# Performance work log

Hardware: AMD Instinct MI355X
Metric: run time of the kernel (lower is better)

## Reference

```python
import jax, jax.numpy as jnp
import numpy as np

B, N, D, H, O = 256, 1024, 512, 2048, 512


def setup_inputs() -> dict:
    key = jax.random.key(0)
    ks = jax.random.split(key, 6)
    x = jax.random.normal(ks[0], (B, N, D), dtype=jnp.float32)
    # binary float mask [B,N,1]; ensure every set has >=1 unpadded element
    mask = (jax.random.uniform(ks[1], (B, N, 1)) < 0.9).astype(jnp.float32)
    mask = mask.at[:, :1, :].set(1.0)
    # per-row (4B rows after stat-concat) unpadded counts in [1, N]
    unpadded = jax.random.randint(ks[2], (4 * B, 1), 1, N + 1).astype(jnp.float32)
    W1 = jax.random.normal(ks[3], (D, H), dtype=jnp.float32) * (1.0 / np.sqrt(D))
    b1 = jnp.zeros((H,), jnp.float32)
    W2 = jax.random.normal(ks[4], (H, O), dtype=jnp.float32) * (1.0 / np.sqrt(H))
    b2 = jnp.zeros((O,), jnp.float32)
    return dict(x=x, mask=mask, unpadded=unpadded, W1=W1, b1=b1, W2=W2, b2=b2)


def reference(x, mask, unpadded, W1, b1, W2, b2):
    # x: [B,N,D], mask: [B,N,1] (0/1 float)
    neg_inf = jnp.float32(-jnp.inf)
    cnt = mask.sum(axis=1)                              # [B,1]
    mean = (x * mask).sum(axis=1) / cnt                 # [B,D]
    agg_max = jnp.where(mask > 0, x, neg_inf).max(axis=1)   # [B,D]
    agg_min = -jnp.where(mask > 0, -x, neg_inf).max(axis=1) # [B,D]
    var = (jnp.square(x - mean[:, None, :]) * mask).sum(axis=1) / cnt
    std = jnp.sqrt(var)                                 # [B,D]
    aggr = jnp.concatenate([mean, agg_max, agg_min, std], axis=0)  # [4B,D]
    # faithful to source: delta = sum(unpadded)/unpadded.shape[1] + 1 (scalar)
    delta = unpadded.sum() / unpadded.shape[1] + 1.0
    logu = jnp.log(unpadded + 1.0)                      # [4B,1]
    amplification = aggr * (logu / delta)
    attenuation = aggr * (delta / logu)
    scale_concat = jnp.concatenate([aggr, amplification, attenuation], axis=0)  # [12B,D]
    h = jax.nn.relu(scale_concat @ W1 + b1)
    return h @ W2 + b2                                  # [12B,O]
```

## Files before the change

kernel.cpp:

```cpp
#include <hip/hip_runtime.h>
#include <hip/hip_bf16.h>
#include <math.h>
#include <stdint.h>

#define B_  256
#define N_  1024
#define D_  512
#define H_  2048
#define O_  512
#define M4  (4 * B_)
#define M12 (12 * B_)
#define NCH 8

typedef __attribute__((ext_vector_type(8))) short short8;
typedef __attribute__((ext_vector_type(4))) float f32x4;
typedef unsigned short ushort_t;

__device__ inline uint32_t pkbf(float a, float b) {
    union { __hip_bfloat162 h; uint32_t u; } cv;
    cv.h = __float22bfloat162_rn(float2{a, b});
    return cv.u;
}
__device__ inline ushort_t f2bf(float f) {
    union { float f; uint32_t u; } v; v.f = f;
    uint32_t r = v.u + 0x7FFFu + ((v.u >> 16) & 1u);
    return (ushort_t)(r >> 16);
}

__device__ inline void load_lds16(const void* g, void* l) {
    typedef const __attribute__((address_space(1))) uint32_t* gp_t;
    typedef __attribute__((address_space(3))) uint32_t* lp_t;
    __builtin_amdgcn_global_load_lds((gp_t)(uintptr_t)g, (lp_t)(uint32_t)(uintptr_t)l,
                                     16, 0, 0);
}

__device__ __forceinline__ void agg_core(const float* __restrict__ x,
                                         const float* __restrict__ mask,
                                         float* __restrict__ part,
                                         float* __restrict__ cntp,
                                         int id, int t) {
    const int b    = id >> 2;
    const int c    = id & 3;
    const int half = t >> 7;
    const int d4   = (t & 127) << 2;
    const float* base = x + ((size_t)b * N_ + (size_t)c * 256) * D_ + d4;
    const float* mp   = mask + (size_t)b * N_ + (size_t)c * 256;

    f32x4 sum = {0.f,0.f,0.f,0.f}, sq = {0.f,0.f,0.f,0.f};
    f32x4 mx = {-INFINITY,-INFINITY,-INFINITY,-INFINITY};
    f32x4 mn = { INFINITY, INFINITY, INFINITY, INFINITY};
    float cnt = 0.f;

    #pragma unroll 8
    for (int n = half; n < 256; n += 2) {
        float m = mp[n];
        f32x4 v = __builtin_nontemporal_load((const f32x4*)(base + (size_t)n * D_));
        sum.x = fmaf(v.x, m, sum.x); sum.y = fmaf(v.y, m, sum.y);
        sum.z = fmaf(v.z, m, sum.z); sum.w = fmaf(v.w, m, sum.w);
        sq.x  = fmaf(v.x * v.x, m, sq.x); sq.y = fmaf(v.y * v.y, m, sq.y);
        sq.z  = fmaf(v.z * v.z, m, sq.z); sq.w = fmaf(v.w * v.w, m, sq.w);
        cnt  += m;
        bool um = m > 0.f;
        mx.x = um ? fmaxf(mx.x, v.x) : mx.x; mx.y = um ? fmaxf(mx.y, v.y) : mx.y;
        mx.z = um ? fmaxf(mx.z, v.z) : mx.z; mx.w = um ? fmaxf(mx.w, v.w) : mx.w;
        mn.x = um ? fminf(mn.x, v.x) : mn.x; mn.y = um ? fminf(mn.y, v.y) : mn.y;
        mn.z = um ? fminf(mn.z, v.z) : mn.z; mn.w = um ? fminf(mn.w, v.w) : mn.w;
    }

    const int ch = c * 2 + half;
    const size_t SS = (size_t)B_ * NCH * D_;
    const size_t pi = ((size_t)(b * NCH + ch)) * D_ + d4;
    *(f32x4*)(part + 0 * SS + pi) = sum;
    *(f32x4*)(part + 1 * SS + pi) = sq;
    *(f32x4*)(part + 2 * SS + pi) = mx;
    *(f32x4*)(part + 3 * SS + pi) = mn;
    if ((t & 127) == 0) cntp[b * NCH + ch] = cnt;
}

__device__ void conv_tile(const float* __restrict__ in, ushort_t* __restrict__ out,
                          int R, int C, int bx, int by, float* tile ) {
    const int t  = threadIdx.x;
    const int r0 = by << 5;
    const int c0 = bx << 5;
    const int tr = t >> 3;
    const int tc = (t & 7) << 2;

    float4 v = *(const float4*)(in + (size_t)(r0 + tr) * C + c0 + tc);
    tile[tr * 33 + tc + 0] = v.x; tile[tr * 33 + tc + 1] = v.y;
    tile[tr * 33 + tc + 2] = v.z; tile[tr * 33 + tc + 3] = v.w;
    __syncthreads();

    union { uint32_t u[2]; ushort4 us; } o;
    o.u[0] = pkbf(tile[(tc + 0) * 33 + tr], tile[(tc + 1) * 33 + tr]);
    o.u[1] = pkbf(tile[(tc + 2) * 33 + tr], tile[(tc + 3) * 33 + tr]);
    *(ushort4*)(out + (size_t)(c0 + tr) * R + r0 + tc) = o.us;
}

__global__ __launch_bounds__(256) void k1_mega(const float* __restrict__ x,
                                               const float* __restrict__ mask,
                                               const float* __restrict__ W1,
                                               const float* __restrict__ W2,
                                               const float* __restrict__ unpadded,
                                               float* __restrict__ part,
                                               float* __restrict__ cntp,
                                               ushort_t* __restrict__ W1t,
                                               ushort_t* __restrict__ W2t,
                                               float* __restrict__ scale) {
    __shared__ float smem[32 * 33];
    const int id = blockIdx.x;
    const int t  = threadIdx.x;

    if (id < 1024) {
        agg_core(x, mask, part, cntp, id, t);
    } else if (id < 2048) {
        const int tid = id - 1024;
        conv_tile(W1, W1t, D_, H_, tid & 63, tid >> 6, smem);
    } else if (id < 3072) {
        const int tid = id - 2048;
        conv_tile(W2, W2t, H_, O_, tid & 15, tid >> 4, smem);
    } else {
        float4 u4 = *(const float4*)(unpadded + t * 4);
        smem[t] = u4.x + u4.y + u4.z + u4.w;
        __syncthreads();
        for (int s = 128; s > 0; s >>= 1) {
            if (t < s) smem[t] += smem[t + s];
            __syncthreads();
        }
        const float delta = smem[0] + 1.0f;
        float uu[4] = {u4.x, u4.y, u4.z, u4.w};
        #pragma unroll
        for (int j = 0; j < 4; ++j) {
            const int i = t * 4 + j;
            const float logu = logf(uu[j] + 1.0f);
            scale[i]          = 1.0f;
            scale[M4 + i]     = logu / delta;
            scale[2 * M4 + i] = delta / logu;
        }
    }
}

__global__ __launch_bounds__(256) void agg_final(const float* __restrict__ part,
                                                 const float* __restrict__ cntp,
                                                 ushort_t* __restrict__ aggr) {
    const int b = blockIdx.x;
    const int t = threadIdx.x;
    const int d = 2 * t;

    float cnt = 0.f;
    #pragma unroll
    for (int c = 0; c < NCH; ++c) cnt += cntp[b * NCH + c];

    const size_t SS = (size_t)B_ * NCH * D_;
    float2 sum = {0.f, 0.f}, sq = {0.f, 0.f};
    float2 mx = {-INFINITY, -INFINITY}, mn = {INFINITY, INFINITY};
    #pragma unroll
    for (int c = 0; c < NCH; ++c) {
        const size_t pi = ((size_t)(b * NCH + c)) * D_ + d;
        float2 s  = *(const float2*)(part + 0 * SS + pi);
        float2 q  = *(const float2*)(part + 1 * SS + pi);
        float2 vx = *(const float2*)(part + 2 * SS + pi);
        float2 vn = *(const float2*)(part + 3 * SS + pi);
        sum.x += s.x; sum.y += s.y;
        sq.x  += q.x; sq.y  += q.y;
        mx.x = fmaxf(mx.x, vx.x); mx.y = fmaxf(mx.y, vx.y);
        mn.x = fminf(mn.x, vn.x); mn.y = fminf(mn.y, vn.y);
    }
    const float ic = 1.f / cnt;
    float2 mean = {sum.x * ic, sum.y * ic};
    float2 var  = {fmaxf(sq.x * ic - mean.x * mean.x, 0.f),
                   fmaxf(sq.y * ic - mean.y * mean.y, 0.f)};

    *(uint32_t*)(aggr + (size_t)(0 * B_ + b) * D_ + d) = pkbf(mean.x, mean.y);
    *(uint32_t*)(aggr + (size_t)(1 * B_ + b) * D_ + d) = pkbf(mx.x, mx.y);
    *(uint32_t*)(aggr + (size_t)(2 * B_ + b) * D_ + d) = pkbf(mn.x, mn.y);
    *(uint32_t*)(aggr + (size_t)(3 * B_ + b) * D_ + d) = pkbf(sqrtf(var.x), sqrtf(var.y));
}

__global__ __launch_bounds__(256) void gemm1_h(const ushort_t* __restrict__ A,
                                               const ushort_t* __restrict__ Bt,
                                               const float* __restrict__ scale,
                                               const float* __restrict__ b1,
                                               ushort_t* __restrict__ h) {
    __shared__ ushort_t As0[64 * 64], As1[64 * 64];
    __shared__ ushort_t Bs0[64 * 64], Bs1[64 * 64];

    const int t    = threadIdx.x;
    const int wave = t >> 6;
    const int lane = t & 63;
    const int wm   = wave >> 1, wn = wave & 1;
    const int row0 = blockIdx.y << 6;
    const int col0 = blockIdx.x << 6;

    const int lr  = lane >> 3;
    const int ksw = ((lane & 7) ^ lr) << 3;

    const int rl = lane & 15;
    const int hi = lane >> 4;

    const ushort_t* Ag0 = A  + (size_t)(row0 + wave * 8 + lr) * D_ + ksw;
    const ushort_t* Ag1 = A  + (size_t)(row0 + 32 + wave * 8 + lr) * D_ + ksw;
    const ushort_t* Bg0 = Bt + (size_t)(col0 + wave * 8 + lr) * D_ + ksw;
    const ushort_t* Bg1 = Bt + (size_t)(col0 + 32 + wave * 8 + lr) * D_ + ksw;
    const int ld0 = (wave * 8) * 64;
    const int ld1 = (32 + wave * 8) * 64;

    f32x4 acc[2][2] = {};

    ushort_t* Ac = As0; ushort_t* An = As1;
    ushort_t* Bc = Bs0; ushort_t* Bn = Bs1;

    load_lds16(Ag0, Ac + ld0); load_lds16(Ag1, Ac + ld1);
    load_lds16(Bg0, Bc + ld0); load_lds16(Bg1, Bc + ld1);
    __syncthreads();

    for (int tt = 0; tt < D_ / 64; ++tt) {
        const int k1 = (tt + 1) * 64;
        if (tt + 1 < D_ / 64) {
            load_lds16(Ag0 + k1, An + ld0); load_lds16(Ag1 + k1, An + ld1);
            load_lds16(Bg0 + k1, Bn + ld0); load_lds16(Bg1 + k1, Bn + ld1);
        }
        short8 av[2][2], bv[2][2];
        #pragma unroll
        for (int i = 0; i < 2; ++i) {
            const int ra = wm * 32 + i * 16 + rl;
            const int rb = wn * 32 + i * 16 + rl;
            #pragma unroll
            for (int k2 = 0; k2 < 2; ++k2) {
                av[i][k2] = *(const short8*)(Ac + ra * 64 + (((k2 * 4 + hi) ^ (ra & 7)) << 3));
                bv[i][k2] = *(const short8*)(Bc + rb * 64 + (((k2 * 4 + hi) ^ (rb & 7)) << 3));
            }
        }
        #pragma unroll
        for (int i = 0; i < 2; ++i)
            #pragma unroll
            for (int j = 0; j < 2; ++j)
                #pragma unroll
                for (int k2 = 0; k2 < 2; ++k2)
                    acc[i][j] = __builtin_amdgcn_mfma_f32_16x16x32_bf16(av[i][k2], bv[j][k2], acc[i][j], 0, 0, 0);
        __syncthreads();
        ushort_t* tp;
        tp = Ac; Ac = An; An = tp;
        tp = Bc; Bc = Bn; Bn = tp;
    }

    #pragma unroll
    for (int i = 0; i < 2; ++i) {
        #pragma unroll
        for (int v = 0; v < 4; ++v) {
            const int row = row0 + wm * 32 + i * 16 + hi * 4 + v;
            const float s1 = scale[M4 + row];
            const float s2 = scale[2 * M4 + row];
            #pragma unroll
            for (int j = 0; j < 2; ++j) {
                const int col = col0 + wn * 32 + j * 16 + rl;
                const float bb = b1[col];
                const float z  = acc[i][j][v];
                h[(size_t)row * H_ + col]            = f2bf(fmaxf(z + bb, 0.f));
                h[(size_t)(M4 + row) * H_ + col]     = f2bf(fmaxf(fmaf(s1, z, bb), 0.f));
                h[(size_t)(2 * M4 + row) * H_ + col] = f2bf(fmaxf(fmaf(s2, z, bb), 0.f));
            }
        }
    }
}

__global__ __launch_bounds__(512) void gemm2_pure(const ushort_t* __restrict__ h,
                                                  const ushort_t* __restrict__ W2t,
                                                  const float* __restrict__ b2,
                                                  float* __restrict__ out) {
    __shared__ ushort_t As[2][2][64 * 64];
    __shared__ ushort_t Bs[2][2][64 * 64];

    const int t    = threadIdx.x;
    const int wave = t >> 6;
    const int kg   = wave >> 2;
    const int w4   = wave & 3;
    const int lane = t & 63;
    const int wm   = w4 >> 1, wn = w4 & 1;

    const int id  = blockIdx.x;
    const int xcd = id & 7;
    const int idx = id >> 3;
    const int rb  = xcd * 6 + (idx % 6);
    const int cb  = idx / 6;
    const int row0 = rb << 6;
    const int col0 = cb << 6;

    const int lr  = lane >> 3;
    const int ksw = ((lane & 7) ^ lr) << 3;
    const int kbase = kg * (H_ / 2);

    const ushort_t* Ag0 = h   + (size_t)(row0 + w4 * 8 + lr) * H_ + kbase + ksw;
    const ushort_t* Ag1 = h   + (size_t)(row0 + 32 + w4 * 8 + lr) * H_ + kbase + ksw;
    const ushort_t* Bg0 = W2t + (size_t)(col0 + w4 * 8 + lr) * H_ + kbase + ksw;
    const ushort_t* Bg1 = W2t + (size_t)(col0 + 32 + w4 * 8 + lr) * H_ + kbase + ksw;
    const int ld0 = (w4 * 8) * 64;
    const int ld1 = (32 + w4 * 8) * 64;

    const int rl = lane & 15;
    const int hi = lane >> 4;

    f32x4 acc[2][2] = {};

    ushort_t* Ac = &As[kg][0][0]; ushort_t* An = &As[kg][1][0];
    ushort_t* Bc = &Bs[kg][0][0]; ushort_t* Bn = &Bs[kg][1][0];

    load_lds16(Ag0, Ac + ld0); load_lds16(Ag1, Ac + ld1);
    load_lds16(Bg0, Bc + ld0); load_lds16(Bg1, Bc + ld1);
    __syncthreads();

    for (int tt = 0; tt < 16; ++tt) {
        const int k1 = (tt + 1) * 64;
        if (tt + 1 < 16) {
            load_lds16(Ag0 + k1, An + ld0); load_lds16(Ag1 + k1, An + ld1);
            load_lds16(Bg0 + k1, Bn + ld0); load_lds16(Bg1 + k1, Bn + ld1);
        }
        short8 av[2][2], bv[2][2];
        #pragma unroll
        for (int i = 0; i < 2; ++i) {
            const int ra = wm * 32 + i * 16 + rl;
            const int rb2 = wn * 32 + i * 16 + rl;
            #pragma unroll
            for (int k2 = 0; k2 < 2; ++k2) {
                av[i][k2] = *(const short8*)(Ac + ra * 64 + (((k2 * 4 + hi) ^ (ra & 7)) << 3));
                bv[i][k2] = *(const short8*)(Bc + rb2 * 64 + (((k2 * 4 + hi) ^ (rb2 & 7)) << 3));
            }
        }
        #pragma unroll
        for (int i = 0; i < 2; ++i)
            #pragma unroll
            for (int j = 0; j < 2; ++j)
                #pragma unroll
                for (int k2 = 0; k2 < 2; ++k2)
                    acc[i][j] = __builtin_amdgcn_mfma_f32_16x16x32_bf16(av[i][k2], bv[j][k2], acc[i][j], 0, 0, 0);
        __syncthreads();
        ushort_t* tp;
        tp = Ac; Ac = An; An = tp;
        tp = Bc; Bc = Bn; Bn = tp;
    }

    float* red = (float*)&As[0][0][0];
    const int fidx = w4 * 1024 + lane * 16;
    if (kg == 1) {
        #pragma unroll
        for (int i = 0; i < 2; ++i)
            #pragma unroll
            for (int j = 0; j < 2; ++j)
                #pragma unroll
                for (int v = 0; v < 4; ++v)
                    red[fidx + i * 8 + j * 4 + v] = acc[i][j][v];
    }
    __syncthreads();
    if (kg == 0) {
        #pragma unroll
        for (int i = 0; i < 2; ++i)
            #pragma unroll
            for (int j = 0; j < 2; ++j) {
                const int col = col0 + wn * 32 + j * 16 + rl;
                const float bb = b2[col];
                #pragma unroll
                for (int v = 0; v < 4; ++v) {
                    const int row = row0 + wm * 32 + i * 16 + hi * 4 + v;
                    out[(size_t)row * O_ + col] =
                        acc[i][j][v] + red[fidx + i * 8 + j * 4 + v] + bb;
                }
            }
    }
}

extern "C" void kernel_launch(void* const* d_in, const int* in_sizes, int n_in,
                              void* d_out, int out_size, void* d_ws, size_t ws_size,
                              hipStream_t stream) {
    const float* x        = (const float*)d_in[0];
    const float* mask     = (const float*)d_in[1];
    const float* unpadded = (const float*)d_in[2];
    const float* W1       = (const float*)d_in[3];
    const float* b1       = (const float*)d_in[4];
    const float* W2       = (const float*)d_in[5];
    const float* b2       = (const float*)d_in[6];
    float* out = (float*)d_out;

    float* ws = (float*)d_ws;
    float* part  = ws;
    float* cntp  = ws + 4194304;
    float* scale = ws + 4196352;
    ushort_t* bfw  = (ushort_t*)(ws + 4200448);
    ushort_t* W1t  = bfw;
    ushort_t* W2t  = bfw + 1048576;
    ushort_t* aggr = bfw + 2097152;
    ushort_t* h    = bfw + 2621440;

    k1_mega<<<3073, 256, 0, stream>>>(x, mask, W1, W2, unpadded,
                                      part, cntp, W1t, W2t, scale);
    agg_final<<<B_, 256, 0, stream>>>(part, cntp, aggr);
    gemm1_h<<<dim3(H_ / 64, M4 / 64), 256, 0, stream>>>(aggr, W1t, scale, b1, h);
    gemm2_pure<<<384, 512, 0, stream>>>(h, W2t, b2, out);
}
```

Baseline: 126.3 us.

## Merge agg_final, gemm1 and gemm2 into one persistent kernel with grid barriers

Replaces the three tail launches (aggregation finalize, first GEMM, second GEMM) with one 512-block kernel that moves between phases through software grid barriers on atomic counters, which are reset by a memset before launch. The goal is to remove kernel launch gaps and tail drain between the phases. The second GEMM is reworked to 256 threads with a split-K of two wave groups and a wider 2x4 MFMA tile per wave. The grid barrier assumes all 512 blocks are co-resident; if they are not, the kernel can deadlock, and the spin adds latency.

```diff
diff --git a/kernel.cpp b/kernel.cpp
--- a/kernel.cpp
+++ b/kernel.cpp
@@ -32,6 +32,17 @@
     typedef __attribute__((address_space(3))) uint32_t* lp_t;
     __builtin_amdgcn_global_load_lds((gp_t)(uintptr_t)g, (lp_t)(uint32_t)(uintptr_t)l,
                                      16, 0, 0);
+}
+
+__device__ inline void gridbar(int* ctr, int target) {
+    __syncthreads();
+    if (threadIdx.x == 0) {
+        __threadfence();
+        atomicAdd(ctr, 1);
+        while (atomicAdd(ctr, 0) < target) __builtin_amdgcn_s_sleep(2);
+        __threadfence();
+    }
+    __syncthreads();
 }
 
 __device__ __forceinline__ void agg_core(const float* __restrict__ x,
@@ -78,7 +89,7 @@
 }
 
 __device__ void conv_tile(const float* __restrict__ in, ushort_t* __restrict__ out,
-                          int R, int C, int bx, int by, float* tile ) {
+                          int R, int C, int bx, int by, float* tile) {
     const int t  = threadIdx.x;
     const int r0 = by << 5;
     const int c0 = bx << 5;
@@ -139,231 +150,235 @@
     }
 }
 
-__global__ __launch_bounds__(256) void agg_final(const float* __restrict__ part,
+__global__ __launch_bounds__(256) void tail_coop(const float* __restrict__ part,
                                                  const float* __restrict__ cntp,
-                                                 ushort_t* __restrict__ aggr) {
-    const int b = blockIdx.x;
-    const int t = threadIdx.x;
-    const int d = 2 * t;
-
-    float cnt = 0.f;
-    #pragma unroll
-    for (int c = 0; c < NCH; ++c) cnt += cntp[b * NCH + c];
-
-    const size_t SS = (size_t)B_ * NCH * D_;
-    float2 sum = {0.f, 0.f}, sq = {0.f, 0.f};
-    float2 mx = {-INFINITY, -INFINITY}, mn = {INFINITY, INFINITY};
-    #pragma unroll
-    for (int c = 0; c < NCH; ++c) {
-        const size_t pi = ((size_t)(b * NCH + c)) * D_ + d;
-        float2 s  = *(const float2*)(part + 0 * SS + pi);
-        float2 q  = *(const float2*)(part + 1 * SS + pi);
-        float2 vx = *(const float2*)(part + 2 * SS + pi);
-        float2 vn = *(const float2*)(part + 3 * SS + pi);
-        sum.x += s.x; sum.y += s.y;
-        sq.x  += q.x; sq.y  += q.y;
-        mx.x = fmaxf(mx.x, vx.x); mx.y = fmaxf(mx.y, vx.y);
-        mn.x = fminf(mn.x, vn.x); mn.y = fminf(mn.y, vn.y);
-    }
-    const float ic = 1.f / cnt;
-    float2 mean = {sum.x * ic, sum.y * ic};
-    float2 var  = {fmaxf(sq.x * ic - mean.x * mean.x, 0.f),
-                   fmaxf(sq.y * ic - mean.y * mean.y, 0.f)};
-
-    *(uint32_t*)(aggr + (size_t)(0 * B_ + b) * D_ + d) = pkbf(mean.x, mean.y);
-    *(uint32_t*)(aggr + (size_t)(1 * B_ + b) * D_ + d) = pkbf(mx.x, mx.y);
-    *(uint32_t*)(aggr + (size_t)(2 * B_ + b) * D_ + d) = pkbf(mn.x, mn.y);
-    *(uint32_t*)(aggr + (size_t)(3 * B_ + b) * D_ + d) = pkbf(sqrtf(var.x), sqrtf(var.y));
-}
-
-__global__ __launch_bounds__(256) void gemm1_h(const ushort_t* __restrict__ A,
-                                               const ushort_t* __restrict__ Bt,
-                                               const float* __restrict__ scale,
-                                               const float* __restrict__ b1,
-                                               ushort_t* __restrict__ h) {
-    __shared__ ushort_t As0[64 * 64], As1[64 * 64];
-    __shared__ ushort_t Bs0[64 * 64], Bs1[64 * 64];
-
+                                                 const float* __restrict__ scale,
+                                                 const float* __restrict__ b1,
+                                                 const ushort_t* __restrict__ W1t,
+                                                 const ushort_t* __restrict__ W2t,
+                                                 const float* __restrict__ b2,
+                                                 ushort_t* __restrict__ aggr,
+                                                 ushort_t* __restrict__ h,
+                                                 float* __restrict__ out,
+                                                 int* __restrict__ bar) {
+    __shared__ char smem_raw[65536];
+    const int id   = blockIdx.x;
     const int t    = threadIdx.x;
     const int wave = t >> 6;
     const int lane = t & 63;
-    const int wm   = wave >> 1, wn = wave & 1;
-    const int row0 = blockIdx.y << 6;
-    const int col0 = blockIdx.x << 6;
-
-    const int lr  = lane >> 3;
-    const int ksw = ((lane & 7) ^ lr) << 3;
-
-    const int rl = lane & 15;
-    const int hi = lane >> 4;
-
-    const ushort_t* Ag0 = A  + (size_t)(row0 + wave * 8 + lr) * D_ + ksw;
-    const ushort_t* Ag1 = A  + (size_t)(row0 + 32 + wave * 8 + lr) * D_ + ksw;
-    const ushort_t* Bg0 = Bt + (size_t)(col0 + wave * 8 + lr) * D_ + ksw;
-    const ushort_t* Bg1 = Bt + (size_t)(col0 + 32 + wave * 8 + lr) * D_ + ksw;
-    const int ld0 = (wave * 8) * 64;
-    const int ld1 = (32 + wave * 8) * 64;
-
-    f32x4 acc[2][2] = {};
-
-    ushort_t* Ac = As0; ushort_t* An = As1;
-    ushort_t* Bc = Bs0; ushort_t* Bn = Bs1;
-
-    load_lds16(Ag0, Ac + ld0); load_lds16(Ag1, Ac + ld1);
-    load_lds16(Bg0, Bc + ld0); load_lds16(Bg1, Bc + ld1);
-    __syncthreads();
-
-    for (int tt = 0; tt < D_ / 64; ++tt) {
-        const int k1 = (tt + 1) * 64;
-        if (tt + 1 < D_ / 64) {
-            load_lds16(Ag0 + k1, An + ld0); load_lds16(Ag1 + k1, An + ld1);
-            load_lds16(Bg0 + k1, Bn + ld0); load_lds16(Bg1 + k1, Bn + ld1);
-        }
-        short8 av[2][2], bv[2][2];
+    const int rl   = lane & 15;
+    const int hi   = lane >> 4;
+    const int lr   = lane >> 3;
+    const int ksw  = ((lane & 7) ^ lr) << 3;
+
+    if (id < 256) {
+        const int b = id;
+        const int d = 2 * t;
+        float cnt = 0.f;
+        #pragma unroll
+        for (int c = 0; c < NCH; ++c) cnt += cntp[b * NCH + c];
+
+        const size_t SS = (size_t)B_ * NCH * D_;
+        float2 sum = {0.f, 0.f}, sq = {0.f, 0.f};
+        float2 mx = {-INFINITY, -INFINITY}, mn = {INFINITY, INFINITY};
+        #pragma unroll
+        for (int c = 0; c < NCH; ++c) {
+            const size_t pi = ((size_t)(b * NCH + c)) * D_ + d;
+            float2 s  = *(const float2*)(part + 0 * SS + pi);
+            float2 q  = *(const float2*)(part + 1 * SS + pi);
+            float2 vx = *(const float2*)(part + 2 * SS + pi);
+            float2 vn = *(const float2*)(part + 3 * SS + pi);
+            sum.x += s.x; sum.y += s.y;
+            sq.x  += q.x; sq.y  += q.y;
+            mx.x = fmaxf(mx.x, vx.x); mx.y = fmaxf(mx.y, vx.y);
+            mn.x = fminf(mn.x, vn.x); mn.y = fminf(mn.y, vn.y);
+        }
+        const float ic = 1.f / cnt;
+        float2 mean = {sum.x * ic, sum.y * ic};
+        float2 var  = {fmaxf(sq.x * ic - mean.x * mean.x, 0.f),
+                       fmaxf(sq.y * ic - mean.y * mean.y, 0.f)};
+
+        *(uint32_t*)(aggr + (size_t)(0 * B_ + b) * D_ + d) = pkbf(mean.x, mean.y);
+        *(uint32_t*)(aggr + (size_t)(1 * B_ + b) * D_ + d) = pkbf(mx.x, mx.y);
+        *(uint32_t*)(aggr + (size_t)(2 * B_ + b) * D_ + d) = pkbf(mn.x, mn.y);
+        *(uint32_t*)(aggr + (size_t)(3 * B_ + b) * D_ + d) = pkbf(sqrtf(var.x), sqrtf(var.y));
+    }
+    gridbar(&bar[0], 512);
+
+    {
+        ushort_t* As0 = (ushort_t*)(smem_raw);
+        ushort_t* As1 = (ushort_t*)(smem_raw + 8192);
+        ushort_t* Bs0 = (ushort_t*)(smem_raw + 16384);
+        ushort_t* Bs1 = (ushort_t*)(smem_raw + 24576);
+
+        const int bx = id & 31;
+        const int by = id >> 5;
+        const int wm = wave >> 1, wn = wave & 1;
+        const int row0 = by << 6;
+        const int col0 = bx << 6;
+
+        const ushort_t* Ag0 = aggr + (size_t)(row0 + wave * 8 + lr) * D_ + ksw;
+        const ushort_t* Ag1 = aggr + (size_t)(row0 + 32 + wave * 8 + lr) * D_ + ksw;
+        const ushort_t* Bg0 = W1t + (size_t)(col0 + wave * 8 + lr) * D_ + ksw;
+        const ushort_t* Bg1 = W1t + (size_t)(col0 + 32 + wave * 8 + lr) * D_ + ksw;
+        const int ld0 = (wave * 8) * 64;
+        const int ld1 = (32 + wave * 8) * 64;
+
+        f32x4 acc[2][2] = {};
+        ushort_t* Ac = As0; ushort_t* An = As1;
+        ushort_t* Bc = Bs0; ushort_t* Bn = Bs1;
+
+        load_lds16(Ag0, Ac + ld0); load_lds16(Ag1, Ac + ld1);
+        load_lds16(Bg0, Bc + ld0); load_lds16(Bg1, Bc + ld1);
+        __syncthreads();
+
+        for (int tt = 0; tt < D_ / 64; ++tt) {
+            const int k1 = (tt + 1) * 64;
+            if (tt + 1 < D_ / 64) {
+                load_lds16(Ag0 + k1, An + ld0); load_lds16(Ag1 + k1, An + ld1);
+                load_lds16(Bg0 + k1, Bn + ld0); load_lds16(Bg1 + k1, Bn + ld1);
+            }
+            short8 av[2][2], bv[2][2];
+            #pragma unroll
+            for (int i = 0; i < 2; ++i) {
+                const int ra = wm * 32 + i * 16 + rl;
+                const int rb = wn * 32 + i * 16 + rl;
+                #pragma unroll
+                for (int k2 = 0; k2 < 2; ++k2) {
+                    av[i][k2] = *(const short8*)(Ac + ra * 64 + (((k2 * 4 + hi) ^ (ra & 7)) << 3));
+                    bv[i][k2] = *(const short8*)(Bc + rb * 64 + (((k2 * 4 + hi) ^ (rb & 7)) << 3));
+                }
+            }
+            #pragma unroll
+            for (int i = 0; i < 2; ++i)
+                #pragma unroll
+                for (int j = 0; j < 2; ++j)
+                    #pragma unroll
+                    for (int k2 = 0; k2 < 2; ++k2)
+                        acc[i][j] = __builtin_amdgcn_mfma_f32_16x16x32_bf16(av[i][k2], bv[j][k2], acc[i][j], 0, 0, 0);
+            __syncthreads();
+            ushort_t* tp;
+            tp = Ac; Ac = An; An = tp;
+            tp = Bc; Bc = Bn; Bn = tp;
+        }
+
         #pragma unroll
         for (int i = 0; i < 2; ++i) {
-            const int ra = wm * 32 + i * 16 + rl;
-            const int rb = wn * 32 + i * 16 + rl;
-            #pragma unroll
-            for (int k2 = 0; k2 < 2; ++k2) {
-                av[i][k2] = *(const short8*)(Ac + ra * 64 + (((k2 * 4 + hi) ^ (ra & 7)) << 3));
-                bv[i][k2] = *(const short8*)(Bc + rb * 64 + (((k2 * 4 + hi) ^ (rb & 7)) << 3));
-            }
-        }
+            #pragma unroll
+            for (int v = 0; v < 4; ++v) {
+                const int row = row0 + wm * 32 + i * 16 + hi * 4 + v;
+                const float s1 = scale[M4 + row];
+                const float s2 = scale[2 * M4 + row];
+                #pragma unroll
+                for (int j = 0; j < 2; ++j) {
+                    const int col = col0 + wn * 32 + j * 16 + rl;
+                    const float bb = b1[col];
+                    const float z  = acc[i][j][v];
+                    h[(size_t)row * H_ + col]            = f2bf(fmaxf(z + bb, 0.f));
+                    h[(size_t)(M4 + row) * H_ + col]     = f2bf(fmaxf(fmaf(s1, z, bb), 0.f));
+                    h[(size_t)(2 * M4 + row) * H_ + col] = f2bf(fmaxf(fmaf(s2, z, bb), 0.f));
+                }
+            }
+        }
+    }
+    gridbar(&bar[1], 512);
+
+    if (id < 384) {
+        const int kg = wave >> 1;
+        const int w2 = wave & 1;
+        const int xcd = id & 7;
+        const int idx = id >> 3;
+        const int rb  = xcd * 6 + (idx % 6);
+        const int cb  = idx / 6;
+        const int row0 = rb << 6;
+        const int col0 = cb << 6;
+        const int kbase = kg * (H_ / 2);
+
+        char* gbase = smem_raw + kg * 32768;
+        ushort_t* Abuf0 = (ushort_t*)(gbase);
+        ushort_t* Abuf1 = (ushort_t*)(gbase + 8192);
+        ushort_t* Bbuf0 = (ushort_t*)(gbase + 16384);
+        ushort_t* Bbuf1 = (ushort_t*)(gbase + 24576);
+
+        const ushort_t* Ag = h   + (size_t)(row0 + w2 * 32 + lr) * H_ + kbase + ksw;
+        const ushort_t* Bg = W2t + (size_t)(col0 + w2 * 32 + lr) * H_ + kbase + ksw;
+        const int lda = (w2 * 32) * 64;
+
+        f32x4 acc[2][4] = {};
+        ushort_t* Ac = Abuf0; ushort_t* An = Abuf1;
+        ushort_t* Bc = Bbuf0; ushort_t* Bn = Bbuf1;
+
         #pragma unroll
-        for (int i = 0; i < 2; ++i)
-            #pragma unroll
-            for (int j = 0; j < 2; ++j)
+        for (int q = 0; q < 4; ++q) {
+            load_lds16(Ag + (size_t)(q * 8) * H_, Ac + lda + q * 8 * 64);
+            load_lds16(Bg + (size_t)(q * 8) * H_, Bc + lda + q * 8 * 64);
+        }
+        __syncthreads();
+
+        for (int tt = 0; tt < 16; ++tt) {
+            const int k1 = (tt + 1) * 64;
+            if (tt + 1 < 16) {
+                #pragma unroll
+                for (int q = 0; q < 4; ++q) {
+                    load_lds16(Ag + (size_t)(q * 8) * H_ + k1, An + lda + q * 8 * 64);
+                    load_lds16(Bg + (size_t)(q * 8) * H_ + k1, Bn + lda + q * 8 * 64);
+                }
+            }
+            short8 av[2][2], bv[4][2];
+            #pragma unroll
+            for (int i = 0; i < 2; ++i) {
+                const int ra = w2 * 32 + i * 16 + rl;
                 #pragma unroll
                 for (int k2 = 0; k2 < 2; ++k2)
-                    acc[i][j] = __builtin_amdgcn_mfma_f32_16x16x32_bf16(av[i][k2], bv[j][k2], acc[i][j], 0, 0, 0);
+                    av[i][k2] = *(const short8*)(Ac + ra * 64 + (((k2 * 4 + hi) ^ (ra & 7)) << 3));
+            }
+            #pragma unroll
+            for (int j = 0; j < 4; ++j) {
+                const int rb2 = j * 16 + rl;
+                #pragma unroll
+                for (int k2 = 0; k2 < 2; ++k2)
+                    bv[j][k2] = *(const short8*)(Bc + rb2 * 64 + (((k2 * 4 + hi) ^ (rb2 & 7)) << 3));
+            }
+            #pragma unroll
+            for (int i = 0; i < 2; ++i)
+                #pragma unroll
+                for (int j = 0; j < 4; ++j)
+                    #pragma unroll
+                    for (int k2 = 0; k2 < 2; ++k2)
+                        acc[i][j] = __builtin_amdgcn_mfma_f32_16x16x32_bf16(av[i][k2], bv[j][k2], acc[i][j], 0, 0, 0);
+            __syncthreads();
+            ushort_t* tp;
+            tp = Ac; Ac = An; An = tp;
+            tp = Bc; Bc = Bn; Bn = tp;
+        }
+
+        float* red = (float*)smem_raw;
+        const int fidx = (w2 * 64 + lane) * 32;
+        if (kg == 1) {
+            #pragma unroll
+            for (int i = 0; i < 2; ++i)
+                #pragma unroll
+                for (int j = 0; j < 4; ++j)
+                    #pragma unroll
+                    for (int v = 0; v < 4; ++v)
+                        red[fidx + i * 16 + j * 4 + v] = acc[i][j][v];
+        }
         __syncthreads();
-        ushort_t* tp;
-        tp = Ac; Ac = An; An = tp;
-        tp = Bc; Bc = Bn; Bn = tp;
-    }
-
-    #pragma unroll
-    for (int i = 0; i < 2; ++i) {
-        #pragma unroll
-        for (int v = 0; v < 4; ++v) {
-            const int row = row0 + wm * 32 + i * 16 + hi * 4 + v;
-            const float s1 = scale[M4 + row];
-            const float s2 = scale[2 * M4 + row];
-            #pragma unroll
-            for (int j = 0; j < 2; ++j) {
-                const int col = col0 + wn * 32 + j * 16 + rl;
-                const float bb = b1[col];
-                const float z  = acc[i][j][v];
-                h[(size_t)row * H_ + col]            = f2bf(fmaxf(z + bb, 0.f));
-                h[(size_t)(M4 + row) * H_ + col]     = f2bf(fmaxf(fmaf(s1, z, bb), 0.f));
-                h[(size_t)(2 * M4 + row) * H_ + col] = f2bf(fmaxf(fmaf(s2, z, bb), 0.f));
-            }
-        }
-    }
-}
-
-__global__ __launch_bounds__(512) void gemm2_pure(const ushort_t* __restrict__ h,
-                                                  const ushort_t* __restrict__ W2t,
-                                                  const float* __restrict__ b2,
-                                                  float* __restrict__ out) {
-    __shared__ ushort_t As[2][2][64 * 64];
-    __shared__ ushort_t Bs[2][2][64 * 64];
-
-    const int t    = threadIdx.x;
-    const int wave = t >> 6;
-    const int kg   = wave >> 2;
-    const int w4   = wave & 3;
-    const int lane = t & 63;
-    const int wm   = w4 >> 1, wn = w4 & 1;
-
-    const int id  = blockIdx.x;
-    const int xcd = id & 7;
-    const int idx = id >> 3;
-    const int rb  = xcd * 6 + (idx % 6);
-    const int cb  = idx / 6;
-    const int row0 = rb << 6;
-    const int col0 = cb << 6;
-
-    const int lr  = lane >> 3;
-    const int ksw = ((lane & 7) ^ lr) << 3;
-    const int kbase = kg * (H_ / 2);
-
-    const ushort_t* Ag0 = h   + (size_t)(row0 + w4 * 8 + lr) * H_ + kbase + ksw;
-    const ushort_t* Ag1 = h   + (size_t)(row0 + 32 + w4 * 8 + lr) * H_ + kbase + ksw;
-    const ushort_t* Bg0 = W2t + (size_t)(col0 + w4 * 8 + lr) * H_ + kbase + ksw;
-    const ushort_t* Bg1 = W2t + (size_t)(col0 + 32 + w4 * 8 + lr) * H_ + kbase + ksw;
-    const int ld0 = (w4 * 8) * 64;
-    const int ld1 = (32 + w4 * 8) * 64;
-
-    const int rl = lane & 15;
-    const int hi = lane >> 4;
-
-    f32x4 acc[2][2] = {};
-
-    ushort_t* Ac = &As[kg][0][0]; ushort_t* An = &As[kg][1][0];
-    ushort_t* Bc = &Bs[kg][0][0]; ushort_t* Bn = &Bs[kg][1][0];
-
-    load_lds16(Ag0, Ac + ld0); load_lds16(Ag1, Ac + ld1);
-    load_lds16(Bg0, Bc + ld0); load_lds16(Bg1, Bc + ld1);
-    __syncthreads();
-
-    for (int tt = 0; tt < 16; ++tt) {
-        const int k1 = (tt + 1) * 64;
-        if (tt + 1 < 16) {
-            load_lds16(Ag0 + k1, An + ld0); load_lds16(Ag1 + k1, An + ld1);
-            load_lds16(Bg0 + k1, Bn + ld0); load_lds16(Bg1 + k1, Bn + ld1);
-        }
-        short8 av[2][2], bv[2][2];
-        #pragma unroll
-        for (int i = 0; i < 2; ++i) {
-            const int ra = wm * 32 + i * 16 + rl;
-            const int rb2 = wn * 32 + i * 16 + rl;
-            #pragma unroll
-            for (int k2 = 0; k2 < 2; ++k2) {
-                av[i][k2] = *(const short8*)(Ac + ra * 64 + (((k2 * 4 + hi) ^ (ra & 7)) << 3));
-                bv[i][k2] = *(const short8*)(Bc + rb2 * 64 + (((k2 * 4 + hi) ^ (rb2 & 7)) << 3));
-            }
-        }
-        #pragma unroll
-        for (int i = 0; i < 2; ++i)
-            #pragma unroll
-            for (int j = 0; j < 2; ++j)
-                #pragma unroll
-                for (int k2 = 0; k2 < 2; ++k2)
-                    acc[i][j] = __builtin_amdgcn_mfma_f32_16x16x32_bf16(av[i][k2], bv[j][k2], acc[i][j], 0, 0, 0);
-        __syncthreads();
-        ushort_t* tp;
-        tp = Ac; Ac = An; An = tp;
-        tp = Bc; Bc = Bn; Bn = tp;
-    }
-
-    float* red = (float*)&As[0][0][0];
-    const int fidx = w4 * 1024 + lane * 16;
-    if (kg == 1) {
-        #pragma unroll
-        for (int i = 0; i < 2; ++i)
-            #pragma unroll
-            for (int j = 0; j < 2; ++j)
-                #pragma unroll
-                for (int v = 0; v < 4; ++v)
-                    red[fidx + i * 8 + j * 4 + v] = acc[i][j][v];
-    }
-    __syncthreads();
-    if (kg == 0) {
-        #pragma unroll
-        for (int i = 0; i < 2; ++i)
-            #pragma unroll
-            for (int j = 0; j < 2; ++j) {
-                const int col = col0 + wn * 32 + j * 16 + rl;
-                const float bb = b2[col];
-                #pragma unroll
-                for (int v = 0; v < 4; ++v) {
-                    const int row = row0 + wm * 32 + i * 16 + hi * 4 + v;
-                    out[(size_t)row * O_ + col] =
-                        acc[i][j][v] + red[fidx + i * 8 + j * 4 + v] + bb;
+        if (kg == 0) {
+            #pragma unroll
+            for (int i = 0; i < 2; ++i)
+                #pragma unroll
+                for (int j = 0; j < 4; ++j) {
+                    const int col = col0 + j * 16 + rl;
+                    const float bb = b2[col];
+                    #pragma unroll
+                    for (int v = 0; v < 4; ++v) {
+                        const int row = row0 + w2 * 32 + i * 16 + hi * 4 + v;
+                        out[(size_t)row * O_ + col] =
+                            acc[i][j][v] + red[fidx + i * 16 + j * 4 + v] + bb;
+                    }
                 }
-            }
+        }
     }
 }
 
@@ -383,15 +398,16 @@
     float* part  = ws;
     float* cntp  = ws + 4194304;
     float* scale = ws + 4196352;
+    int*   bar   = (int*)(ws + 4199424);
     ushort_t* bfw  = (ushort_t*)(ws + 4200448);
     ushort_t* W1t  = bfw;
     ushort_t* W2t  = bfw + 1048576;
     ushort_t* aggr = bfw + 2097152;
     ushort_t* h    = bfw + 2621440;
 
+    hipMemsetAsync(bar, 0, 64, stream);
     k1_mega<<<3073, 256, 0, stream>>>(x, mask, W1, W2, unpadded,
                                       part, cntp, W1t, W2t, scale);
-    agg_final<<<B_, 256, 0, stream>>>(part, cntp, aggr);
-    gemm1_h<<<dim3(H_ / 64, M4 / 64), 256, 0, stream>>>(aggr, W1t, scale, b1, h);
-    gemm2_pure<<<384, 512, 0, stream>>>(h, W2t, b2, out);
-}
+    tail_coop<<<512, 256, 0, stream>>>(part, cntp, scale, b1, W1t, W2t, b2,
+                                       aggr, h, out, bar);
+}
```

Result: slower. 235.1 us (+86.1%).
